# Kernel optimization log

Measured on AMD Instinct MI355X. Metric: run time of the kernel, lower is better.

Reference implementation:

```python
import jax, jax.numpy as jnp
import numpy as np

B, S, D, H, NL = 4, 1024, 512, 8, 2
DFF = 4 * D
EPS = 1e-5


def _layernorm(x, g, b):
    m = x.mean(-1, keepdims=True)
    v = ((x - m) ** 2).mean(-1, keepdims=True)
    return (x - m) / jnp.sqrt(v + EPS) * g + b


def _forward(x, Wq, bq, Wk, bk, Wv, bv, Wo, bo, W1, b1, W2, b2, ln1_g, ln1_b, ln2_g, ln2_b):
    Bn, Sn, Dn = x.shape
    Nl, Hh = Wq.shape[0], Wq.shape[1]
    dk = Dn // Hh  # scaling uses dmodel//h even though heads are full-width (faithful to SDPA)
    for i in range(Nl):
        # per-head full-width projections: each head maps dmodel -> dmodel
        q = jnp.einsum('bsd,hed->bhse', x, Wq[i]) + bq[i][:, None, :]
        k = jnp.einsum('bsd,hed->bhse', x, Wk[i]) + bk[i][:, None, :]
        v = jnp.einsum('bsd,hed->bhse', x, Wv[i]) + bv[i][:, None, :]
        scores = jnp.einsum('bhse,bhte->bhst', q, k) / jnp.sqrt(jnp.asarray(dk, x.dtype))
        attn = jax.nn.softmax(scores, axis=-1)
        heads = jnp.einsum('bhst,bhte->bhse', attn, v)          # [B,H,S,D]
        cat = heads.transpose(0, 2, 1, 3).reshape(Bn, Sn, Hh * Dn)  # concat heads -> [B,S,H*D]
        mha_out = cat @ Wo[i].T + bo[i]
        x = _layernorm(x + mha_out, ln1_g[i], ln1_b[i])
        ff = jax.nn.relu(x @ W1[i].T + b1[i]) @ W2[i].T + b2[i]
        x = _layernorm(x + ff, ln2_g[i], ln2_b[i])
    return x


def setup_inputs() -> dict:
    key = jax.random.key(0)
    ks = jax.random.split(key, 12)
    def w(k, shape, fan_in):
        return (jax.random.normal(k, shape, jnp.float32) / np.sqrt(fan_in)).astype(jnp.float32)
    inp = {
        'x': jax.random.normal(ks[0], (B, S, D), jnp.float32),
        'Wq': w(ks[1], (NL, H, D, D), D), 'bq': jnp.zeros((NL, H, D), jnp.float32),
        'Wk': w(ks[2], (NL, H, D, D), D), 'bk': jnp.zeros((NL, H, D), jnp.float32),
        'Wv': w(ks[3], (NL, H, D, D), D), 'bv': jnp.zeros((NL, H, D), jnp.float32),
        'Wo': w(ks[4], (NL, D, H * D), H * D), 'bo': jnp.zeros((NL, D), jnp.float32),
        'W1': w(ks[5], (NL, DFF, D), D), 'b1': jnp.zeros((NL, DFF), jnp.float32),
        'W2': w(ks[6], (NL, D, DFF), DFF), 'b2': jnp.zeros((NL, D), jnp.float32),
        'ln1_g': jnp.ones((NL, D), jnp.float32), 'ln1_b': jnp.zeros((NL, D), jnp.float32),
        'ln2_g': jnp.ones((NL, D), jnp.float32), 'ln2_b': jnp.zeros((NL, D), jnp.float32),
    }
    return inp


def reference(x, Wq, bq, Wk, bk, Wv, bv, Wo, bo, W1, b1, W2, b2, ln1_g, ln1_b, ln2_g, ln2_b):
    return _forward(x, Wq, bq, Wk, bk, Wv, bv, Wo, bo, W1, b1, W2, b2, ln1_g, ln1_b, ln2_g, ln2_b)
```

## Files before the change

kernel.cpp:

```cpp
#include <hip/hip_runtime.h>
#include <cstdint>
#include <cstddef>

#define NB 4
#define NS 1024
#define ND 512
#define NH 8
#define NLAYER 2
#define NDFF 2048

typedef __attribute__((ext_vector_type(8))) short short8;
typedef __attribute__((ext_vector_type(4))) float f32x4;
typedef __attribute__((ext_vector_type(4))) unsigned short u16x4;
typedef unsigned short u16;
typedef long long ll;

__device__ __forceinline__ float b2f(u16 u) {
  union { unsigned int i; float f; } x; x.i = ((unsigned int)u) << 16; return x.f;
}
__device__ __forceinline__ u16 f2b(float f) {
  union { float f; unsigned int i; } x; x.f = f;
  return (u16)((x.i + 0x7FFF + ((x.i >> 16) & 1)) >> 16);
}

struct Zm { int div; ll hi, lo; };
__device__ __forceinline__ ll zoff(Zm m, int z) {
  return (ll)(z / m.div) * m.hi + (ll)(z % m.div) * m.lo;
}

enum { F_BF16 = 1, F_RELU = 2, F_BCOL = 4, F_BROW = 8, F_RESID = 16 };

__device__ __forceinline__ void load_lds16(const void* g, void* s) {
  __builtin_amdgcn_global_load_lds(
      (const __attribute__((address_space(1))) void*)(uintptr_t)g,
      (__attribute__((address_space(3))) void*)(uint32_t)(uintptr_t)s, 16, 0, 0);
}

#define MFMA16(d, a, b) \
  asm volatile("v_mfma_f32_16x16x32_bf16 %0, %1, %2, %0" : "+v"(d) : "v"(a), "v"(b))

__global__ void __launch_bounds__(256)
gemm_bt(const u16* __restrict__ A, int lda, Zm za,
        const u16* __restrict__ Bw, int ldb, Zm zb,
        const u16* __restrict__ Bw2, const float* __restrict__ bias2, int zsplit,
        void* __restrict__ Cv, int ldc, Zm zc,
        const float* __restrict__ bias, Zm zbias,
        const float* __restrict__ resid,
        float scale, int K, int flags)
{
  __shared__ __align__(16) char smem[2][16384];

  const int gx = gridDim.x, gy = gridDim.y;
  int id = (blockIdx.z * gy + blockIdx.y) * gx + blockIdx.x;
  const int nwg = gx * gy * (int)gridDim.z;
  if ((nwg & 7) == 0) id = (id & 7) * (nwg >> 3) + (id >> 3);
  const int bx = id % gx;
  const int rest = id / gx;
  const int by = rest % gy;
  const int z0 = rest / gy;

  int zB = z0;
  const u16* Bsel = Bw;
  const float* bsel = bias;
  if (z0 >= zsplit) { Bsel = Bw2; bsel = bias2; zB = z0 - zsplit; }

  A    += zoff(za, z0);
  Bsel += zoff(zb, zB);

  const int bm = by * 128, bn = bx * 128;
  const int t = threadIdx.x;
  const int w = t >> 6, lane = t & 63;
  const int wr = w >> 1, wc = w & 1;

  const u16* ga0 = A    + (size_t)(bm + (t >> 2)) * lda + ((t & 3) << 3);
  const u16* ga1 = ga0 + (size_t)64 * lda;
  const u16* gb0 = Bsel + (size_t)(bn + (t >> 2)) * ldb + ((t & 3) << 3);
  const u16* gb1 = gb0 + (size_t)64 * ldb;

  auto STAGE = [&](int sel, int kt) {
    const int k0 = kt << 5;
    char* sa = smem[sel] + (w << 10);
    char* sb = smem[sel] + 8192 + (w << 10);
    load_lds16(ga0 + k0, sa);
    load_lds16(ga1 + k0, sa + 4096);
    load_lds16(gb0 + k0, sb);
    load_lds16(gb1 + k0, sb + 4096);
  };

  f32x4 acc[4][4];
#pragma unroll
  for (int i = 0; i < 4; ++i)
#pragma unroll
    for (int j = 0; j < 4; ++j) acc[i][j] = (f32x4){0.f, 0.f, 0.f, 0.f};

  const int fr = lane & 15;
  const int kg = (lane >> 4) << 3;

  const int nt = K >> 5;
  STAGE(0, 0);
  __syncthreads();
  int cur = 0;
  for (int kt = 0; kt < nt; ++kt) {
    if (kt + 1 < nt) STAGE(cur ^ 1, kt + 1);
    const u16* la = (const u16*)smem[cur];
    const u16* lb = (const u16*)(smem[cur] + 8192);
    short8 af[4], bf[4];
#pragma unroll
    for (int mi = 0; mi < 4; ++mi)
      af[mi] = *(const short8*)(la + (wr * 64 + mi * 16 + fr) * 32 + kg);
#pragma unroll
    for (int ni = 0; ni < 4; ++ni)
      bf[ni] = *(const short8*)(lb + (wc * 64 + ni * 16 + fr) * 32 + kg);
#pragma unroll
    for (int mi = 0; mi < 4; ++mi)
#pragma unroll
      for (int ni = 0; ni < 4; ++ni)
        MFMA16(acc[mi][ni], af[mi], bf[ni]);
    __syncthreads();
    cur ^= 1;
  }

  asm volatile("s_nop 7\n\ts_nop 7" ::: "memory");

  const ll co = zoff(zc, z0);
  const float* bz = (flags & (F_BCOL | F_BROW)) ? bsel + zoff(zbias, zB) : nullptr;
  const int r0 = (lane >> 4) << 2;
  const int c0 = lane & 15;
#pragma unroll
  for (int mi = 0; mi < 4; ++mi) {
#pragma unroll
    for (int ni = 0; ni < 4; ++ni) {
#pragma unroll
      for (int r = 0; r < 4; ++r) {
        const int grow = bm + wr * 64 + mi * 16 + r0 + r;
        const int gcol = bn + wc * 64 + ni * 16 + c0;
        float v = acc[mi][ni][r] * scale;
        if (flags & F_BCOL) v += bz[gcol];
        if (flags & F_BROW) v += bz[grow];
        if (flags & F_RELU) v = fmaxf(v, 0.f);
        if (flags & F_RESID) v += resid[(size_t)grow * ldc + gcol];
        const ll idx = co + (ll)grow * ldc + gcol;
        if (flags & F_BF16) ((u16*)Cv)[idx] = f2b(v);
        else                ((float*)Cv)[idx] = v;
      }
    }
  }
}

__global__ void __launch_bounds__(256, 2)
fattn(const u16* __restrict__ qg, const u16* __restrict__ kg,
      const u16* __restrict__ vtg, u16* __restrict__ cat)
{
  __shared__ __align__(16) u16 kv_lds[128 * 128];
  __shared__ __align__(16) u16 p_lds[64 * 136];

  int id = blockIdx.x;
  id = (id & 7) * 64 + (id >> 3);
  const int qt = id & 15;
  const int hb = id >> 4;
  const int h = hb >> 2, b = hb & 3;

  const ll hbase = (ll)h * NB * NS * ND;
  const u16* Q  = qg  + hbase + ((ll)(b * NS + qt * 64)) * ND;
  const u16* Kp = kg  + hbase + (ll)b * NS * ND;
  const u16* VT = vtg + (ll)hb * ND * NS;
  u16* Op = cat + ((ll)(b * NS + qt * 64)) * (NH * ND) + h * ND;

  const int t = threadIdx.x;
  const int w = t >> 6, lane = t & 63;
  const int fr = lane & 15, khi = lane >> 4;

  short8 qreg[16];
#pragma unroll
  for (int s = 0; s < 16; ++s)
    qreg[s] = *(const short8*)(Q + (ll)(w * 16 + fr) * ND + s * 32 + khi * 8);

  const int srow = t >> 4;
  const int scol = (((t & 15) ^ (srow & 7)) << 3);
  char* const qkb = (char*)kv_lds;
  const int wslab = w << 10;

  f32x4 o[4][8];
#pragma unroll
  for (int ec = 0; ec < 4; ++ec)
#pragma unroll
    for (int nf = 0; nf < 8; ++nf) o[ec][nf] = (f32x4){0.f, 0.f, 0.f, 0.f};
  float m_r[4] = {-1e30f, -1e30f, -1e30f, -1e30f};
  float l_r[4] = {0.f, 0.f, 0.f, 0.f};

  for (int kv = 0; kv < 8; ++kv) {
    f32x4 s[8];
#pragma unroll
    for (int nf = 0; nf < 8; ++nf) s[nf] = (f32x4){0.f, 0.f, 0.f, 0.f};

    for (int dch = 0; dch < 4; ++dch) {
#pragma unroll
      for (int i = 0; i < 8; ++i)
        load_lds16(Kp + (ll)(kv * 128 + i * 16 + srow) * ND + dch * 128 + scol,
                   qkb + i * 4096 + wslab);
      __syncthreads();
#pragma unroll
      for (int ks = 0; ks < 4; ++ks) {
        const short8 aq = qreg[dch * 4 + ks];
        const int gq = (((4 * ks + khi) ^ (fr & 7)) << 3);
#pragma unroll
        for (int nf = 0; nf < 8; ++nf) {
          short8 bk = *(const short8*)(kv_lds + (nf * 16 + fr) * 128 + gq);
          MFMA16(s[nf], aq, bk);
        }
      }
      __syncthreads();
    }
    asm volatile("s_nop 7\n\ts_nop 7" ::: "memory");

    float mxs[4];
    bool big = false;
#pragma unroll
    for (int r = 0; r < 4; ++r) {
      float mx = s[0][r];
#pragma unroll
      for (int nf = 1; nf < 8; ++nf) mx = fmaxf(mx, s[nf][r]);
      mx *= 0.125f;
      mx = fmaxf(mx, __shfl_xor(mx, 1));
      mx = fmaxf(mx, __shfl_xor(mx, 2));
      mx = fmaxf(mx, __shfl_xor(mx, 4));
      mx = fmaxf(mx, __shfl_xor(mx, 8));
      mxs[r] = mx;
      big = big || (mx > m_r[r] + 8.f);
    }
    const bool resc = __any(big);
    float f_r[4];
#pragma unroll
    for (int r = 0; r < 4; ++r) {
      const float mn = resc ? fmaxf(m_r[r], mxs[r]) : m_r[r];
      f_r[r] = resc ? __expf(m_r[r] - mn) : 1.f;
      m_r[r] = mn;
      float sum = 0.f;
#pragma unroll
      for (int nf = 0; nf < 8; ++nf) {
        const float e = __expf(s[nf][r] * 0.125f - mn);
        sum += e;
        p_lds[(w * 16 + 4 * khi + r) * 136 + nf * 16 + fr] = f2b(e);
      }
      sum += __shfl_xor(sum, 1);
      sum += __shfl_xor(sum, 2);
      sum += __shfl_xor(sum, 4);
      sum += __shfl_xor(sum, 8);
      l_r[r] = l_r[r] * f_r[r] + sum;
    }
    if (resc) {
#pragma unroll
      for (int ec = 0; ec < 4; ++ec)
#pragma unroll
        for (int nf = 0; nf < 8; ++nf)
#pragma unroll
          for (int r = 0; r < 4; ++r) o[ec][nf][r] *= f_r[r];
    }

    asm volatile("s_waitcnt lgkmcnt(0)" ::: "memory");
    __builtin_amdgcn_sched_barrier(0);
    short8 ap[4];
#pragma unroll
    for (int ks = 0; ks < 4; ++ks)
      ap[ks] = *(const short8*)(p_lds + (w * 16 + fr) * 136 + 32 * ks + 8 * khi);

#pragma unroll
    for (int ec = 0; ec < 4; ++ec) {
#pragma unroll
      for (int i = 0; i < 8; ++i)
        load_lds16(VT + (ll)(ec * 128 + i * 16 + srow) * NS + kv * 128 + scol,
                   qkb + i * 4096 + wslab);
      __syncthreads();
#pragma unroll
      for (int ks = 0; ks < 4; ++ks) {
        const int gv = (((4 * ks + khi) ^ (fr & 7)) << 3);
#pragma unroll
        for (int nf = 0; nf < 8; ++nf) {
          short8 bv8 = *(const short8*)(kv_lds + (nf * 16 + fr) * 128 + gv);
          MFMA16(o[ec][nf], ap[ks], bv8);
        }
      }
      __syncthreads();
    }
  }

  asm volatile("s_nop 7\n\ts_nop 7" ::: "memory");
#pragma unroll
  for (int r = 0; r < 4; ++r) {
    const float inv = 1.f / l_r[r];
    const ll row = (ll)(w * 16 + 4 * khi + r) * (NH * ND);
#pragma unroll
    for (int ec = 0; ec < 4; ++ec)
#pragma unroll
      for (int nf = 0; nf < 8; ++nf)
        Op[row + ec * 128 + nf * 16 + fr] = f2b(o[ec][nf][r] * inv);
  }
}

__global__ void __launch_bounds__(256)
ln_red(const float* __restrict__ parts, int np, ll pstride,
       const float* __restrict__ bias, const float* __restrict__ resid,
       const float* __restrict__ g, const float* __restrict__ be,
       float* __restrict__ xout, u16* __restrict__ xbout)
{
  const int t = threadIdx.x, w = t >> 6, lane = t & 63;
  const ll row = (ll)blockIdx.x * 4 + w;
  const ll base = row * ND + lane * 8;
  float v[8];
  *(f32x4*)(v)     = *(const f32x4*)(resid + base);
  *(f32x4*)(v + 4) = *(const f32x4*)(resid + base + 4);
#pragma unroll
  for (int j = 0; j < 8; ++j) v[j] += bias[lane * 8 + j];
  for (int pIdx = 0; pIdx < np; ++pIdx) {
    const float* pp = parts + pIdx * pstride + base;
    f32x4 a0 = *(const f32x4*)(pp);
    f32x4 a1 = *(const f32x4*)(pp + 4);
    v[0] += a0.x; v[1] += a0.y; v[2] += a0.z; v[3] += a0.w;
    v[4] += a1.x; v[5] += a1.y; v[6] += a1.z; v[7] += a1.w;
  }
  float s = 0.f, q = 0.f;
#pragma unroll
  for (int j = 0; j < 8; ++j) { s += v[j]; q += v[j] * v[j]; }
#pragma unroll
  for (int o = 32; o >= 1; o >>= 1) { s += __shfl_xor(s, o); q += __shfl_xor(q, o); }
  const float mean = s * (1.f / ND);
  const float var  = q * (1.f / ND) - mean * mean;
  const float inv  = 1.f / sqrtf(var + 1e-5f);
#pragma unroll
  for (int j = 0; j < 8; ++j) {
    const int c = lane * 8 + j;
    const float y = (v[j] - mean) * inv * g[c] + be[c];
    xout[row * ND + c] = y;
    xbout[row * ND + c] = f2b(y);
  }
}

struct CvtJobs { const float* src[7]; u16* dst[7]; ll n[7]; };

__global__ void __launch_bounds__(256)
cvt7(CvtJobs j)
{
  const int z = blockIdx.y;
  const ll i = ((ll)blockIdx.x * 256 + threadIdx.x) * 4;
  if (i >= j.n[z]) return;
  f32x4 v = *(const f32x4*)(j.src[z] + i);
  u16x4 o;
  o.x = f2b(v.x); o.y = f2b(v.y); o.z = f2b(v.z); o.w = f2b(v.w);
  *(u16x4*)(j.dst[z] + i) = o;
}

extern "C" void kernel_launch(void* const* d_in, const int* in_sizes, int n_in,
                              void* d_out, int out_size, void* d_ws, size_t ws_size,
                              hipStream_t stream)
{
  (void)in_sizes; (void)n_in; (void)out_size; (void)ws_size;
  const float* x_in = (const float*)d_in[0];
  const float* Wq = (const float*)d_in[1];  const float* bq = (const float*)d_in[2];
  const float* Wk = (const float*)d_in[3];  const float* bk = (const float*)d_in[4];
  const float* Wv = (const float*)d_in[5];  const float* bv = (const float*)d_in[6];
  const float* Wo = (const float*)d_in[7];  const float* bo = (const float*)d_in[8];
  const float* W1 = (const float*)d_in[9];  const float* b1 = (const float*)d_in[10];
  const float* W2 = (const float*)d_in[11]; const float* b2 = (const float*)d_in[12];
  const float* ln1g = (const float*)d_in[13]; const float* ln1b = (const float*)d_in[14];
  const float* ln2g = (const float*)d_in[15]; const float* ln2b = (const float*)d_in[16];

  char* p = (char*)d_ws;
  auto alloc = [&](ll bytes) { char* r = p; p += (bytes + 255) & ~(ll)255; return r; };
  const ll nWq = (ll)NLAYER * NH * ND * ND;
  const ll nWo = (ll)NLAYER * ND * NH * ND;
  const ll nW1 = (ll)NLAYER * NDFF * ND;
  const ll nX  = (ll)NB * NS * ND;

  u16* wq_b = (u16*)alloc(nWq * 2);
  u16* wk_b = (u16*)alloc(nWq * 2);
  u16* wv_b = (u16*)alloc(nWq * 2);
  u16* wo_b = (u16*)alloc(nWo * 2);
  u16* w1_b = (u16*)alloc(nW1 * 2);
  u16* w2_b = (u16*)alloc(nW1 * 2);
  u16* xb   = (u16*)alloc(nX * 2);
  u16* qb   = (u16*)alloc((ll)NH * NB * NS * ND * 2);
  u16* kb   = (u16*)alloc((ll)NH * NB * NS * ND * 2);
  u16* vT   = (u16*)alloc((ll)NH * NB * ND * NS * 2);
  u16* scb  = (u16*)alloc((ll)NB * NH * NS * NS * 2);
  u16* cat = scb;
  float* parts = (float*)(scb + (ll)NB * NS * NH * ND);
  u16* ffh = qb;

  CvtJobs cj;
  cj.src[0] = Wq; cj.dst[0] = wq_b; cj.n[0] = nWq;
  cj.src[1] = Wk; cj.dst[1] = wk_b; cj.n[1] = nWq;
  cj.src[2] = Wv; cj.dst[2] = wv_b; cj.n[2] = nWq;
  cj.src[3] = Wo; cj.dst[3] = wo_b; cj.n[3] = nWo;
  cj.src[4] = W1; cj.dst[4] = w1_b; cj.n[4] = nW1;
  cj.src[5] = W2; cj.dst[5] = w2_b; cj.n[5] = nW1;
  cj.src[6] = x_in; cj.dst[6] = xb; cj.n[6] = nX;
  cvt7<<<dim3((unsigned)((nWq / 4 + 255) / 256), 7), 256, 0, stream>>>(cj);

  float* xf = (float*)d_out;
  const Zm Z0{1, 0, 0};
  const ll PSTR = nX;
  const int ZINF = 1 << 30;

  for (int i = 0; i < NLAYER; ++i) {
    const float* resid1 = (i == 0) ? x_in : xf;
    const ll woff = (ll)i * NH * ND * ND;

    gemm_bt<<<dim3(ND/128, (NB*NS)/128, 2*NH), 256, 0, stream>>>(
        xb, ND, Z0,
        wq_b + woff, ND, Zm{1, (ll)ND * ND, 0},
        wk_b + woff, bk + (ll)i * NH * ND, NH,
        qb, ND, Zm{1, (ll)NB * NS * ND, 0},
        bq + (ll)i * NH * ND, Zm{1, ND, 0}, nullptr, 1.f, ND, F_BF16 | F_BCOL);

    gemm_bt<<<dim3(NS/128, ND/128, NH*NB), 256, 0, stream>>>(
        wv_b + woff, ND, Zm{NB, (ll)ND * ND, 0},
        xb, ND, Zm{NB, 0, (ll)NS * ND},
        xb, nullptr, ZINF,
        vT, NS, Zm{1, (ll)ND * NS, 0},
        bv + (ll)i * NH * ND, Zm{NB, ND, 0}, nullptr, 1.f, ND, F_BF16 | F_BROW);

    fattn<<<dim3(512), 256, 0, stream>>>(qb, kb, vT, cat);

    gemm_bt<<<dim3(ND/128, (NB*NS)/128, 4), 256, 0, stream>>>(
        cat, NH * ND, Zm{1, 1024, 0},
        wo_b + (ll)i * ND * NH * ND, NH * ND, Zm{1, 1024, 0},
        wo_b, nullptr, ZINF,
        parts, ND, Zm{1, PSTR, 0},
        nullptr, Z0, nullptr, 1.f, 1024, 0);

    ln_red<<<dim3(NB * NS / 4), 256, 0, stream>>>(
        parts, 4, PSTR, bo + (ll)i * ND, resid1,
        ln1g + (ll)i * ND, ln1b + (ll)i * ND, xf, xb);

    gemm_bt<<<dim3(NDFF/128, (NB*NS)/128, 1), 256, 0, stream>>>(
        xb, ND, Z0,
        w1_b + (ll)i * NDFF * ND, ND, Z0,
        w1_b, nullptr, ZINF,
        ffh, NDFF, Z0,
        b1 + (ll)i * NDFF, Z0, nullptr, 1.f, ND, F_BF16 | F_BCOL | F_RELU);

    gemm_bt<<<dim3(ND/128, (NB*NS)/128, 4), 256, 0, stream>>>(
        ffh, NDFF, Zm{1, 512, 0},
        w2_b + (ll)i * ND * NDFF, NDFF, Zm{1, 512, 0},
        w2_b, nullptr, ZINF,
        parts, ND, Zm{1, PSTR, 0},
        nullptr, Z0, nullptr, 1.f, 512, 0);

    ln_red<<<dim3(NB * NS / 4), 256, 0, stream>>>(
        parts, 4, PSTR, b2 + (ll)i * ND, xf,
        ln2g + (ll)i * ND, ln2b + (ll)i * ND, xf, xb);
  }
}
```

Baseline: 672.6 us.

## Double-buffer K/V LDS tiles in flash attention to overlap loads with MFMA

The attention kernel gets two LDS buffers for K and V^T tiles. A single staging routine walks the combined K-chunk and V-chunk sequence and prefetches the next tile into the other buffer while MFMAs consume the current one. This removes the exposed global-to-LDS latency before each chunk and one barrier per step. LDS use per block grows to about 80KB, which limits occupancy. The padding on the P scratch rows is also dropped (stride 136 to 128), which may add LDS bank conflicts when P is read back.

```diff
diff --git a/kernel.cpp b/kernel.cpp
--- a/kernel.cpp
+++ b/kernel.cpp
@@ -151,8 +151,8 @@
 fattn(const u16* __restrict__ qg, const u16* __restrict__ kg,
       const u16* __restrict__ vtg, u16* __restrict__ cat)
 {
-  __shared__ __align__(16) u16 kv_lds[128 * 128];
-  __shared__ __align__(16) u16 p_lds[64 * 136];
+  __shared__ __align__(16) u16 kv_lds[2][128 * 128];
+  __shared__ __align__(16) u16 p_lds[64 * 128];
 
   int id = blockIdx.x;
   id = (id & 7) * 64 + (id >> 3);
@@ -177,8 +177,25 @@
 
   const int srow = t >> 4;
   const int scol = (((t & 15) ^ (srow & 7)) << 3);
-  char* const qkb = (char*)kv_lds;
   const int wslab = w << 10;
+
+  auto STG = [&](int g) {
+    const int kv2 = g >> 3, ph = g & 7;
+    if (kv2 >= 8) return;
+    char* dst = (char*)kv_lds[g & 1];
+    if (ph < 4) {
+#pragma unroll
+      for (int i = 0; i < 8; ++i)
+        load_lds16(Kp + (ll)(kv2 * 128 + i * 16 + srow) * ND + ph * 128 + scol,
+                   dst + i * 4096 + wslab);
+    } else {
+      const int ec = ph - 4;
+#pragma unroll
+      for (int i = 0; i < 8; ++i)
+        load_lds16(VT + (ll)(ec * 128 + i * 16 + srow) * NS + kv2 * 128 + scol,
+                   dst + i * 4096 + wslab);
+    }
+  };
 
   f32x4 o[4][8];
 #pragma unroll
@@ -188,24 +205,26 @@
   float m_r[4] = {-1e30f, -1e30f, -1e30f, -1e30f};
   float l_r[4] = {0.f, 0.f, 0.f, 0.f};
 
+  STG(0);
+  __syncthreads();
+
   for (int kv = 0; kv < 8; ++kv) {
     f32x4 s[8];
 #pragma unroll
     for (int nf = 0; nf < 8; ++nf) s[nf] = (f32x4){0.f, 0.f, 0.f, 0.f};
 
+#pragma unroll
     for (int dch = 0; dch < 4; ++dch) {
-#pragma unroll
-      for (int i = 0; i < 8; ++i)
-        load_lds16(Kp + (ll)(kv * 128 + i * 16 + srow) * ND + dch * 128 + scol,
-                   qkb + i * 4096 + wslab);
-      __syncthreads();
+      const int g = kv * 8 + dch;
+      STG(g + 1);
+      const u16* kb_ = kv_lds[g & 1];
 #pragma unroll
       for (int ks = 0; ks < 4; ++ks) {
         const short8 aq = qreg[dch * 4 + ks];
         const int gq = (((4 * ks + khi) ^ (fr & 7)) << 3);
 #pragma unroll
         for (int nf = 0; nf < 8; ++nf) {
-          short8 bk = *(const short8*)(kv_lds + (nf * 16 + fr) * 128 + gq);
+          short8 bk = *(const short8*)(kb_ + (nf * 16 + fr) * 128 + gq);
           MFMA16(s[nf], aq, bk);
         }
       }
@@ -240,7 +259,7 @@
       for (int nf = 0; nf < 8; ++nf) {
         const float e = __expf(s[nf][r] * 0.125f - mn);
         sum += e;
-        p_lds[(w * 16 + 4 * khi + r) * 136 + nf * 16 + fr] = f2b(e);
+        p_lds[(w * 16 + 4 * khi + r) * 128 + nf * 16 + fr] = f2b(e);
       }
       sum += __shfl_xor(sum, 1);
       sum += __shfl_xor(sum, 2);
@@ -262,21 +281,19 @@
     short8 ap[4];
 #pragma unroll
     for (int ks = 0; ks < 4; ++ks)
-      ap[ks] = *(const short8*)(p_lds + (w * 16 + fr) * 136 + 32 * ks + 8 * khi);
+      ap[ks] = *(const short8*)(p_lds + (w * 16 + fr) * 128 + 32 * ks + 8 * khi);
 
 #pragma unroll
     for (int ec = 0; ec < 4; ++ec) {
-#pragma unroll
-      for (int i = 0; i < 8; ++i)
-        load_lds16(VT + (ll)(ec * 128 + i * 16 + srow) * NS + kv * 128 + scol,
-                   qkb + i * 4096 + wslab);
-      __syncthreads();
+      const int g = kv * 8 + 4 + ec;
+      STG(g + 1);
+      const u16* vb = kv_lds[g & 1];
 #pragma unroll
       for (int ks = 0; ks < 4; ++ks) {
         const int gv = (((4 * ks + khi) ^ (fr & 7)) << 3);
 #pragma unroll
         for (int nf = 0; nf < 8; ++nf) {
-          short8 bv8 = *(const short8*)(kv_lds + (nf * 16 + fr) * 128 + gv);
+          short8 bv8 = *(const short8*)(vb + (nf * 16 + fr) * 128 + gv);
           MFMA16(o[ec][nf], ap[ks], bv8);
         }
       }
```

New measurement: 739.5 us. 1.1x slower.
